# Performance work log

Measured on AMD Instinct MI355X. Metric: run time of the kernel, lower is better.

## Reference

```python
import jax, jax.numpy as jnp
import numpy as np

B, S, H = 4, 2048, 1024

def setup_inputs() -> dict:
    key = jax.random.key(0)
    ks = jax.random.split(key, 4)
    scale = 1.0 / np.sqrt(H)
    x = jax.random.normal(ks[0], (B, S, H), dtype=jnp.float32)
    Wq = jax.random.normal(ks[1], (H, H), dtype=jnp.float32) * scale
    Wk = jax.random.normal(ks[2], (H, H), dtype=jnp.float32) * scale
    Wv = jax.random.normal(ks[3], (H, H), dtype=jnp.float32) * scale
    bq = jnp.zeros((H,), dtype=jnp.float32)
    bk = jnp.zeros((H,), dtype=jnp.float32)
    bv = jnp.zeros((H,), dtype=jnp.float32)
    return {"x": x, "Wq": Wq, "bq": bq, "Wk": Wk, "bk": bk, "Wv": Wv, "bv": bv}

def reference(x, Wq, bq, Wk, bk, Wv, bv):
    # Linear: y = x @ W^T + b (torch nn.Linear convention)
    Q = jnp.einsum('bsh,oh->bso', x, Wq) + bq
    K = jnp.einsum('bsh,oh->bso', x, Wk) + bk
    V = jnp.einsum('bsh,oh->bso', x, Wv) + bv
    scores = jnp.einsum('bqh,bkh->bqk', Q, K) / jnp.sqrt(jnp.float32(H))
    attn = jax.nn.softmax(scores, axis=-1)
    return jnp.einsum('bqk,bkh->bqh', attn, V)
```

## Files before the change

kernel.cpp:

```cpp
#include <hip/hip_runtime.h>
#include <cstdint>
#include <cstddef>


typedef __bf16 bf16;
typedef _Float16 f16;
typedef __bf16 bf16x8 __attribute__((ext_vector_type(8)));
typedef __bf16 bf16x4 __attribute__((ext_vector_type(4)));
typedef _Float16 f16x8 __attribute__((ext_vector_type(8)));
typedef float f32x4 __attribute__((ext_vector_type(4)));

#define LDS_TOTAL 131072

#define XQ (8388608 / 4)
#define WQ (1048576 / 4)
__global__ __launch_bounds__(256)
void cvt_all(const float* __restrict__ x, const float* __restrict__ Wq,
             const float* __restrict__ Wk, const float* __restrict__ Wv,
             bf16* __restrict__ xb, bf16* __restrict__ Wqkv)
{
    const int i = blockIdx.x * 256 + threadIdx.x;
    const float* src;
    bf16* dst;
    if (i < XQ) {
        src = x + 4 * (size_t)i;
        dst = xb + 4 * (size_t)i;
    } else {
        const int j = i - XQ;
        const int w = j / WQ;
        const int off = j - w * WQ;
        const float* ws_ = (w == 0) ? Wq : (w == 1) ? Wk : Wv;
        src = ws_ + 4 * (size_t)off;
        dst = Wqkv + 4 * (size_t)j;
    }
    f32x4 v = *(const f32x4*)src;
    bf16x4 o;
#pragma unroll
    for (int r = 0; r < 4; ++r) o[r] = (bf16)v[r];
    *(bf16x4*)dst = o;
}

#define BM1 128
#define BN1 128
#define BK1 64

__device__ __forceinline__ void stage_tile(const bf16* __restrict__ g, int ld,
                                           bf16* lds_generic, int tid)
{
    auto lds3 = (__attribute__((address_space(3))) char*)lds_generic;
    const int wave = tid >> 6;
#pragma unroll
    for (int issue = 0; issue < 4; ++issue) {
        const int p   = issue * 256 + tid;
        const int row = p >> 3;
        const int cp  = p & 7;
        const int c   = cp ^ (row & 7);
        const bf16* gp = g + (size_t)row * ld + c * 8;
        const unsigned wave_base = (unsigned)(issue * 4096 + wave * 1024);
        __builtin_amdgcn_global_load_lds(
            (const __attribute__((address_space(1))) void*)gp,
            (__attribute__((address_space(3))) void*)(lds3 + wave_base),
            16, 0, 0);
    }
}

__device__ __forceinline__ bf16x8 read_frag(const bf16* lds, int row, int chunk)
{
    const int cp = chunk ^ (row & 7);
    return *(const bf16x8*)(lds + row * BK1 + cp * 8);
}

template <int OUTMODE, int DBUF>
__global__ __launch_bounds__(256, DBUF ? 2 : 4)
void gemm_bt(const bf16* __restrict__ A, const bf16* __restrict__ Bm,
             const float* __restrict__ bias0, const float* __restrict__ bias1,
             const float* __restrict__ bias2, void* __restrict__ C,
             int K, int N, float alpha, long zA, long zB, long zC)
{
    __shared__ alignas(16) bf16 As[DBUF + 1][BM1 * BK1];
    __shared__ alignas(16) bf16 Bs[DBUF + 1][BN1 * BK1];

    const int tid  = threadIdx.x;
    const int lane = tid & 63;
    const int wid  = tid >> 6;
    const int wr   = (wid >> 1) * 64;
    const int wc   = (wid & 1) * 64;
    const int quad = lane >> 4;
    const int l16  = lane & 15;

    const int m0 = blockIdx.y * BM1;
    const int n0 = blockIdx.x * BN1;
    const int z  = blockIdx.z;

    const bf16* Ab = A + (size_t)z * zA + (size_t)m0 * K;
    const bf16* Bb = Bm + (size_t)z * zB + (size_t)n0 * K;

    f32x4 acc[4][4] = {};

    if (DBUF) {
        stage_tile(Ab, K, As[0], tid);
        stage_tile(Bb, K, Bs[0], tid);
    }

    const int niter = K / BK1;
    for (int it = 0; it < niter; ++it) {
        int cur;
        if (DBUF) {
            cur = it & 1;
            __syncthreads();
            if (it + 1 < niter) {
                stage_tile(Ab + (it + 1) * BK1, K, As[cur ^ 1], tid);
                stage_tile(Bb + (it + 1) * BK1, K, Bs[cur ^ 1], tid);
            }
        } else {
            cur = 0;
            __syncthreads();
            stage_tile(Ab + it * BK1, K, As[0], tid);
            stage_tile(Bb + it * BK1, K, Bs[0], tid);
            __syncthreads();
        }
#pragma unroll
        for (int h = 0; h < 2; ++h) {
            bf16x8 af[4], bfr[4];
#pragma unroll
            for (int i = 0; i < 4; ++i)
                af[i]  = read_frag(As[cur], wr + i * 16 + l16, h * 4 + quad);
#pragma unroll
            for (int j = 0; j < 4; ++j)
                bfr[j] = read_frag(Bs[cur], wc + j * 16 + l16, h * 4 + quad);

#pragma unroll
            for (int i = 0; i < 4; ++i)
#pragma unroll
                for (int j = 0; j < 4; ++j)
                    acc[i][j] = __builtin_amdgcn_mfma_f32_16x16x32_bf16(
                        af[i], bfr[j], acc[i][j], 0, 0, 0);
        }
    }

#pragma unroll
    for (int j = 0; j < 4; ++j) {
        const int col3 = n0 + wc + j * 16 + l16;
#pragma unroll
        for (int i = 0; i < 4; ++i) {
            const int rbase = m0 + wr + i * 16 + quad * 4;
            const int mat = col3 >> 10;
            const int col = col3 & 1023;
            const float* bp = (mat == 0) ? bias0 : (mat == 1) ? bias1 : bias2;
            const float bj = bp[col];
            if (mat < 2) {
                bf16* Cb = (bf16*)C + (size_t)mat * (8u << 20);
#pragma unroll
                for (int r = 0; r < 4; ++r)
                    Cb[(size_t)(rbase + r) * 1024 + col] =
                        (bf16)(acc[i][j][r] + bj);
            } else {
                bf16* Cb = (bf16*)C + (size_t)(16u << 20);
                const int b = rbase >> 11;
                const int s = rbase & 2047;
                bf16x4 tmp;
#pragma unroll
                for (int r = 0; r < 4; ++r) tmp[r] = (bf16)(acc[i][j][r] + bj);
                *(bf16x4*)(Cb + (((size_t)((b << 10) + col)) << 11) + s) = tmp;
            }
        }
    }
}

template <int OUTMODE, int NW_N>
__global__ __launch_bounds__(512, 2)
void gemm256(const bf16* __restrict__ A, const bf16* __restrict__ Bm,
             void* __restrict__ C,
             int K, int N, float alpha, long zA, long zB, long zC)
{
    constexpr int MI = 2 * NW_N;
    extern __shared__ __align__(16) char smem[];
    auto lds3 = (__attribute__((address_space(3))) char*)smem;

    const int tid  = threadIdx.x;
    const int lane = tid & 63;
    const int wid  = tid >> 6;
    const int quad = lane >> 4;
    const int l16  = lane & 15;
    const int wc   = (wid % NW_N) * 64;
    const int wr   = (wid / NW_N) * (MI * 16);

    const unsigned gx = gridDim.x, gy = gridDim.y;
    unsigned flat = blockIdx.x + gx * (blockIdx.y + gy * blockIdx.z);
    const unsigned chunk = (gx * gy * gridDim.z) >> 3;
    flat = (flat & 7u) * chunk + (flat >> 3);
    const int bx = flat % gx;
    const unsigned r2 = flat / gx;
    const int by = r2 % gy;
    const int z  = r2 / gy;

    const int m0 = by * 256;
    const int n0 = bx * (NW_N * 64);

    const bf16* Ab = A + (size_t)z * zA + (size_t)m0 * K;
    const bf16* Bb = Bm + (size_t)z * zB + (size_t)n0 * K;

    const int sr  = tid >> 3;
    const int sc  = (tid & 7) ^ (sr & 7);
    const size_t soff = (size_t)sr * K + (size_t)sc * 8;
    const long  hstep = 64L * K;
    const long  h1off = 128L * K;
    const unsigned dmabase = (unsigned)(wid * 1024);

#define STAGE(g, ldsoff)                                                       \
    do {                                                                       \
        __builtin_amdgcn_global_load_lds(                                      \
            (const __attribute__((address_space(1))) void*)((g) + soff),       \
            (__attribute__((address_space(3))) void*)(lds3 + (ldsoff) + dmabase), \
            16, 0, 0);                                                         \
        __builtin_amdgcn_global_load_lds(                                      \
            (const __attribute__((address_space(1))) void*)((g) + soff + hstep), \
            (__attribute__((address_space(3))) void*)(lds3 + (ldsoff) + 8192 + dmabase), \
            16, 0, 0);                                                         \
    } while (0)

    const char* pa = (const char*)smem + (wr + l16) * 128;
    const int x0 = (quad ^ (l16 & 7)) * 16;

    const int NT = K / 64;
    f32x4 acc[MI][4] = {};

    if constexpr (NW_N == 4) {
        const char* pb = (const char*)smem + 65536 + (wc + l16) * 128;
        bf16x8 af[4][2], b01[2][2], b23[2][2];

        STAGE(Ab, 0u);           STAGE(Ab + h1off, 16384u);
        STAGE(Bb, 65536u);       STAGE(Bb + h1off, 65536u + 16384u);
        STAGE(Ab + 64, 32768u);  STAGE(Ab + 64 + h1off, 32768u + 16384u);
        asm volatile("s_waitcnt vmcnt(4)\n\ts_barrier" ::: "memory");

        for (int t = 0; t < NT; ++t) {
            const unsigned d  = (unsigned)(t & 1) * 32768u;
            const unsigned dn = 32768u - d;
            const char* paT = pa + d;
            const char* pbT = pb + d;

#pragma unroll
            for (int i = 0; i < 4; ++i) {
                af[i][0] = *(const bf16x8*)(paT + i * 2048 + x0);
                af[i][1] = *(const bf16x8*)(paT + i * 2048 + (x0 ^ 64));
            }
#pragma unroll
            for (int j = 0; j < 2; ++j) {
                b01[j][0] = *(const bf16x8*)(pbT + j * 2048 + x0);
                b01[j][1] = *(const bf16x8*)(pbT + j * 2048 + (x0 ^ 64));
            }
            if (t + 1 < NT) STAGE(Bb + (t + 1) * 64, 65536u + dn);
            __builtin_amdgcn_s_setprio(1);
#pragma unroll
            for (int i = 0; i < 4; ++i)
#pragma unroll
                for (int j = 0; j < 2; ++j) {
                    acc[i][j] = __builtin_amdgcn_mfma_f32_16x16x32_bf16(
                        af[i][0], b01[j][0], acc[i][j], 0, 0, 0);
                    acc[i][j] = __builtin_amdgcn_mfma_f32_16x16x32_bf16(
                        af[i][1], b01[j][1], acc[i][j], 0, 0, 0);
                }
            __builtin_amdgcn_s_setprio(0);

#pragma unroll
            for (int j = 0; j < 2; ++j) {
                b23[j][0] = *(const bf16x8*)(pbT + (2 + j) * 2048 + x0);
                b23[j][1] = *(const bf16x8*)(pbT + (2 + j) * 2048 + (x0 ^ 64));
            }
            if (t + 1 < NT) STAGE(Bb + (t + 1) * 64 + h1off, 65536u + dn + 16384u);
            __builtin_amdgcn_s_setprio(1);
#pragma unroll
            for (int i = 0; i < 4; ++i)
#pragma unroll
                for (int j = 0; j < 2; ++j) {
                    acc[i][2 + j] = __builtin_amdgcn_mfma_f32_16x16x32_bf16(
                        af[i][0], b23[j][0], acc[i][2 + j], 0, 0, 0);
                    acc[i][2 + j] = __builtin_amdgcn_mfma_f32_16x16x32_bf16(
                        af[i][1], b23[j][1], acc[i][2 + j], 0, 0, 0);
                }
            __builtin_amdgcn_s_setprio(0);

#pragma unroll
            for (int i = 0; i < 4; ++i) {
                af[i][0] = *(const bf16x8*)(paT + (4 + i) * 2048 + x0);
                af[i][1] = *(const bf16x8*)(paT + (4 + i) * 2048 + (x0 ^ 64));
            }
            __builtin_amdgcn_s_setprio(1);
#pragma unroll
            for (int i = 0; i < 4; ++i)
#pragma unroll
                for (int j = 0; j < 2; ++j) {
                    acc[4 + i][2 + j] = __builtin_amdgcn_mfma_f32_16x16x32_bf16(
                        af[i][0], b23[j][0], acc[4 + i][2 + j], 0, 0, 0);
                    acc[4 + i][2 + j] = __builtin_amdgcn_mfma_f32_16x16x32_bf16(
                        af[i][1], b23[j][1], acc[4 + i][2 + j], 0, 0, 0);
                }
            __builtin_amdgcn_s_setprio(0);

            asm volatile("s_barrier" ::: "memory");

#pragma unroll
            for (int j = 0; j < 2; ++j) {
                b01[j][0] = *(const bf16x8*)(pbT + j * 2048 + x0);
                b01[j][1] = *(const bf16x8*)(pbT + j * 2048 + (x0 ^ 64));
            }
            if (t + 2 < NT) {
                STAGE(Ab + (t + 2) * 64, d);
                STAGE(Ab + (t + 2) * 64 + h1off, d + 16384u);
            }
            __builtin_amdgcn_s_setprio(1);
#pragma unroll
            for (int i = 0; i < 4; ++i)
#pragma unroll
                for (int j = 0; j < 2; ++j) {
                    acc[4 + i][j] = __builtin_amdgcn_mfma_f32_16x16x32_bf16(
                        af[i][0], b01[j][0], acc[4 + i][j], 0, 0, 0);
                    acc[4 + i][j] = __builtin_amdgcn_mfma_f32_16x16x32_bf16(
                        af[i][1], b01[j][1], acc[4 + i][j], 0, 0, 0);
                }
            __builtin_amdgcn_s_setprio(0);

            if (t + 2 < NT)
                asm volatile("s_waitcnt vmcnt(4)\n\ts_barrier" ::: "memory");
            else if (t + 1 < NT)
                asm volatile("s_waitcnt vmcnt(0)\n\ts_barrier" ::: "memory");
        }
    } else {
        bf16x8 af[2][2], bfr[4][2];

        STAGE(Ab, 0u);           STAGE(Ab + h1off, 16384u);
        STAGE(Bb, 98304u);
        STAGE(Ab + 64, 32768u);  STAGE(Ab + 64 + h1off, 32768u + 16384u);
        asm volatile("s_waitcnt vmcnt(4)\n\ts_barrier" ::: "memory");

        for (int t = 0; t < NT; ++t) {
            const char* paT = pa + (unsigned)(t % 3) * 32768u;
            const char* pbT = (const char*)smem + 98304u +
                              (unsigned)(t & 1) * 16384u + (wc + l16) * 128;

#pragma unroll
            for (int i = 0; i < 2; ++i) {
                af[i][0] = *(const bf16x8*)(paT + i * 2048 + x0);
                af[i][1] = *(const bf16x8*)(paT + i * 2048 + (x0 ^ 64));
            }
#pragma unroll
            for (int j = 0; j < 4; ++j) {
                bfr[j][0] = *(const bf16x8*)(pbT + j * 2048 + x0);
                bfr[j][1] = *(const bf16x8*)(pbT + j * 2048 + (x0 ^ 64));
            }
            if (t + 1 < NT)
                STAGE(Bb + (t + 1) * 64, 98304u + (unsigned)((t + 1) & 1) * 16384u);
            __builtin_amdgcn_s_setprio(1);
#pragma unroll
            for (int i = 0; i < 2; ++i)
#pragma unroll
                for (int j = 0; j < 4; ++j) {
                    acc[i][j] = __builtin_amdgcn_mfma_f32_16x16x32_bf16(
                        af[i][0], bfr[j][0], acc[i][j], 0, 0, 0);
                    acc[i][j] = __builtin_amdgcn_mfma_f32_16x16x32_bf16(
                        af[i][1], bfr[j][1], acc[i][j], 0, 0, 0);
                }
            __builtin_amdgcn_s_setprio(0);

#pragma unroll
            for (int i = 0; i < 2; ++i) {
                af[i][0] = *(const bf16x8*)(paT + (2 + i) * 2048 + x0);
                af[i][1] = *(const bf16x8*)(paT + (2 + i) * 2048 + (x0 ^ 64));
            }
            if (t + 2 < NT) {
                const unsigned da = (unsigned)((t + 2) % 3) * 32768u;
                STAGE(Ab + (t + 2) * 64, da);
                STAGE(Ab + (t + 2) * 64 + h1off, da + 16384u);
            }
            __builtin_amdgcn_s_setprio(1);
#pragma unroll
            for (int i = 0; i < 2; ++i)
#pragma unroll
                for (int j = 0; j < 4; ++j) {
                    acc[2 + i][j] = __builtin_amdgcn_mfma_f32_16x16x32_bf16(
                        af[i][0], bfr[j][0], acc[2 + i][j], 0, 0, 0);
                    acc[2 + i][j] = __builtin_amdgcn_mfma_f32_16x16x32_bf16(
                        af[i][1], bfr[j][1], acc[2 + i][j], 0, 0, 0);
                }
            __builtin_amdgcn_s_setprio(0);

            if (t + 2 < NT)
                asm volatile("s_waitcnt vmcnt(4)\n\ts_barrier" ::: "memory");
            else if (t + 1 < NT)
                asm volatile("s_waitcnt vmcnt(0)\n\ts_barrier" ::: "memory");
        }
    }
#undef STAGE

#pragma unroll
    for (int j = 0; j < 4; ++j) {
        const int col3 = n0 + wc + j * 16 + l16;
#pragma unroll
        for (int i = 0; i < MI; ++i) {
            const int rbase = m0 + wr + i * 16 + quad * 4;
            if (OUTMODE == 2) {
                f16* Cf = (f16*)C + (size_t)z * zC;
#pragma unroll
                for (int r = 0; r < 4; ++r)
                    Cf[(size_t)(rbase + r) * N + col3] = (f16)(acc[i][j][r] * alpha);
            } else {
                float* Cf = (float*)C + (size_t)z * zC;
#pragma unroll
                for (int r = 0; r < 4; ++r)
                    Cf[(size_t)(rbase + r) * N + col3] = acc[i][j][r];
            }
        }
    }
}

__device__ __forceinline__ float wred_max(float v)
{
#pragma unroll
    for (int o = 32; o > 0; o >>= 1) v = fmaxf(v, __shfl_xor(v, o, 64));
    return v;
}
__device__ __forceinline__ float wred_sum(float v)
{
#pragma unroll
    for (int o = 32; o > 0; o >>= 1) v += __shfl_xor(v, o, 64);
    return v;
}

__global__ __launch_bounds__(256)
void softmax_rows(const f16* __restrict__ Sc, bf16* __restrict__ P)
{
    constexpr int NC = 2048;
    const size_t row = blockIdx.x;
    const f16* src = Sc + row * NC;
    bf16* dst = P + row * NC;
    const int tid = threadIdx.x;

    f16x8 in = *(const f16x8*)(src + tid * 8);
    float v[8];
    float m = -3.4e38f;
#pragma unroll
    for (int i = 0; i < 8; ++i) {
        v[i] = (float)in[i];
        m = fmaxf(m, v[i]);
    }
    m = wred_max(m);

    __shared__ float redm[4], reds[4];
    if ((tid & 63) == 0) redm[tid >> 6] = m;
    __syncthreads();
    m = fmaxf(fmaxf(redm[0], redm[1]), fmaxf(redm[2], redm[3]));

    float s = 0.f;
#pragma unroll
    for (int i = 0; i < 8; ++i) { v[i] = __expf(v[i] - m); s += v[i]; }
    s = wred_sum(s);
    if ((tid & 63) == 0) reds[tid >> 6] = s;
    __syncthreads();
    s = reds[0] + reds[1] + reds[2] + reds[3];

    const float inv = 1.f / s;
    bf16x8 o;
#pragma unroll
    for (int i = 0; i < 8; ++i) o[i] = (bf16)(v[i] * inv);
    *(bf16x8*)(dst + tid * 8) = o;
}

extern "C" void kernel_launch(void* const* d_in, const int* in_sizes, int n_in,
                              void* d_out, int out_size, void* d_ws, size_t ws_size,
                              hipStream_t stream)
{
    constexpr int B = 4, S = 2048, H = 1024;
    const float* x  = (const float*)d_in[0];
    const float* Wq = (const float*)d_in[1];
    const float* bq = (const float*)d_in[2];
    const float* Wk = (const float*)d_in[3];
    const float* bk = (const float*)d_in[4];
    const float* Wv = (const float*)d_in[5];
    const float* bv = (const float*)d_in[6];
    float* out = (float*)d_out;

    char* ws = (char*)d_ws;
    bf16* xb   = (bf16*)ws;
    bf16* Wqkv = (bf16*)(ws + (size_t)(16 << 20));
    bf16* Q    = (bf16*)(ws + (size_t)(22 << 20));
    bf16* Kp   = (bf16*)(ws + (size_t)(38 << 20));
    bf16* Vt   = (bf16*)(ws + (size_t)(54 << 20));
    f16*  Sc   = (f16*) (ws + (size_t)(70 << 20));
    bf16* P    = (bf16*)(ws + (size_t)(22 << 20));

    static bool attr_done = false;
    if (!attr_done) {
        attr_done = true;
        (void)hipFuncSetAttribute(reinterpret_cast<const void*>(gemm256<2, 4>),
                                  hipFuncAttributeMaxDynamicSharedMemorySize,
                                  LDS_TOTAL);
        (void)hipFuncSetAttribute(reinterpret_cast<const void*>(gemm256<3, 2>),
                                  hipFuncAttributeMaxDynamicSharedMemorySize,
                                  LDS_TOTAL);
    }

    dim3 blk(256, 1, 1);
    dim3 blk512(512, 1, 1);

    cvt_all<<<dim3((XQ + 3 * WQ) / 256), blk, 0, stream>>>(
        x, Wq, Wk, Wv, xb, Wqkv);

    gemm_bt<4, 1><<<dim3(3 * H / BN1, (B * S) / BM1, 1), blk, 0, stream>>>(
        xb, Wqkv, bq, bk, bv, Q, H, 3 * H, 1.0f, 0, 0, 0);

    gemm256<2, 4><<<dim3(S / 256, S / 256, B), blk512, LDS_TOTAL, stream>>>(
        Q, Kp, Sc, H, S, 0.03125f,
        (long)S * H, (long)S * H, (long)S * S);

    softmax_rows<<<dim3(B * S), blk, 0, stream>>>(Sc, P);

    gemm256<3, 2><<<dim3(H / 128, S / 256, B), blk512, LDS_TOTAL, stream>>>(
        P, Vt, out, S, H, 1.0f,
        (long)S * S, (long)H * S, (long)S * H);
}
```

Before: 245.3 us.

## Fuse softmax normalization into PV GEMM using precomputed row statistics

The separate softmax kernel that wrote a bf16 probability matrix is replaced by a stats kernel that only computes per-row max and inverse sum. The PV GEMM then loads raw f16 scores, applies exp and normalization in registers, and writes bf16 into LDS before the MFMA loop, with a two-stage buffer. This removes the write and re-read of the full P matrix. The cost is that the exp work is repeated for every column tile of the PV GEMM (8 tiles over H), and A-operand staging becomes register-mediated rather than a direct global-to-LDS DMA. The GEMM templates are also specialized into dedicated kernels.

```diff
diff --git a/kernel.cpp b/kernel.cpp
--- a/kernel.cpp
+++ b/kernel.cpp
@@ -10,7 +10,8 @@
 typedef _Float16 f16x8 __attribute__((ext_vector_type(8)));
 typedef float f32x4 __attribute__((ext_vector_type(4)));
 
-#define LDS_TOTAL 131072
+#define LDS_GEMM256 131072
+#define LDS_PV       98304
 
 #define XQ (8388608 / 4)
 #define WQ (1048576 / 4)
@@ -70,15 +71,13 @@
     return *(const bf16x8*)(lds + row * BK1 + cp * 8);
 }
 
-template <int OUTMODE, int DBUF>
-__global__ __launch_bounds__(256, DBUF ? 2 : 4)
-void gemm_bt(const bf16* __restrict__ A, const bf16* __restrict__ Bm,
-             const float* __restrict__ bias0, const float* __restrict__ bias1,
-             const float* __restrict__ bias2, void* __restrict__ C,
-             int K, int N, float alpha, long zA, long zB, long zC)
-{
-    __shared__ alignas(16) bf16 As[DBUF + 1][BM1 * BK1];
-    __shared__ alignas(16) bf16 Bs[DBUF + 1][BN1 * BK1];
+__global__ __launch_bounds__(256, 2)
+void gemm_qkv(const bf16* __restrict__ A, const bf16* __restrict__ Bm,
+              const float* __restrict__ bias0, const float* __restrict__ bias1,
+              const float* __restrict__ bias2, bf16* __restrict__ C, int K)
+{
+    __shared__ alignas(16) bf16 As[2][BM1 * BK1];
+    __shared__ alignas(16) bf16 Bs[2][BN1 * BK1];
 
     const int tid  = threadIdx.x;
     const int lane = tid & 63;
@@ -90,34 +89,22 @@
 
     const int m0 = blockIdx.y * BM1;
     const int n0 = blockIdx.x * BN1;
-    const int z  = blockIdx.z;
-
-    const bf16* Ab = A + (size_t)z * zA + (size_t)m0 * K;
-    const bf16* Bb = Bm + (size_t)z * zB + (size_t)n0 * K;
+
+    const bf16* Ab = A + (size_t)m0 * K;
+    const bf16* Bb = Bm + (size_t)n0 * K;
 
     f32x4 acc[4][4] = {};
 
-    if (DBUF) {
-        stage_tile(Ab, K, As[0], tid);
-        stage_tile(Bb, K, Bs[0], tid);
-    }
+    stage_tile(Ab, K, As[0], tid);
+    stage_tile(Bb, K, Bs[0], tid);
 
     const int niter = K / BK1;
     for (int it = 0; it < niter; ++it) {
-        int cur;
-        if (DBUF) {
-            cur = it & 1;
-            __syncthreads();
-            if (it + 1 < niter) {
-                stage_tile(Ab + (it + 1) * BK1, K, As[cur ^ 1], tid);
-                stage_tile(Bb + (it + 1) * BK1, K, Bs[cur ^ 1], tid);
-            }
-        } else {
-            cur = 0;
-            __syncthreads();
-            stage_tile(Ab + it * BK1, K, As[0], tid);
-            stage_tile(Bb + it * BK1, K, Bs[0], tid);
-            __syncthreads();
+        const int cur = it & 1;
+        __syncthreads();
+        if (it + 1 < niter) {
+            stage_tile(Ab + (it + 1) * BK1, K, As[cur ^ 1], tid);
+            stage_tile(Bb + (it + 1) * BK1, K, Bs[cur ^ 1], tid);
         }
 #pragma unroll
         for (int h = 0; h < 2; ++h) {
@@ -128,7 +115,6 @@
 #pragma unroll
             for (int j = 0; j < 4; ++j)
                 bfr[j] = read_frag(Bs[cur], wc + j * 16 + l16, h * 4 + quad);
-
 #pragma unroll
             for (int i = 0; i < 4; ++i)
 #pragma unroll
@@ -149,13 +135,13 @@
             const float* bp = (mat == 0) ? bias0 : (mat == 1) ? bias1 : bias2;
             const float bj = bp[col];
             if (mat < 2) {
-                bf16* Cb = (bf16*)C + (size_t)mat * (8u << 20);
+                bf16* Cb = C + (size_t)mat * (8u << 20);
 #pragma unroll
                 for (int r = 0; r < 4; ++r)
                     Cb[(size_t)(rbase + r) * 1024 + col] =
                         (bf16)(acc[i][j][r] + bj);
             } else {
-                bf16* Cb = (bf16*)C + (size_t)(16u << 20);
+                bf16* Cb = C + (size_t)(16u << 20);
                 const int b = rbase >> 11;
                 const int s = rbase & 2047;
                 bf16x4 tmp;
@@ -167,13 +153,11 @@
     }
 }
 
-template <int OUTMODE, int NW_N>
 __global__ __launch_bounds__(512, 2)
-void gemm256(const bf16* __restrict__ A, const bf16* __restrict__ Bm,
-             void* __restrict__ C,
-             int K, int N, float alpha, long zA, long zB, long zC)
-{
-    constexpr int MI = 2 * NW_N;
+void gemm_scores(const bf16* __restrict__ A, const bf16* __restrict__ Bm,
+                 f16* __restrict__ C, int K, int N, float alpha,
+                 long zA, long zB, long zC)
+{
     extern __shared__ __align__(16) char smem[];
     auto lds3 = (__attribute__((address_space(3))) char*)smem;
 
@@ -182,8 +166,8 @@
     const int wid  = tid >> 6;
     const int quad = lane >> 4;
     const int l16  = lane & 15;
-    const int wc   = (wid % NW_N) * 64;
-    const int wr   = (wid / NW_N) * (MI * 16);
+    const int wc   = (wid & 3) * 64;
+    const int wr   = (wid >> 2) * 128;
 
     const unsigned gx = gridDim.x, gy = gridDim.y;
     unsigned flat = blockIdx.x + gx * (blockIdx.y + gy * blockIdx.z);
@@ -195,7 +179,7 @@
     const int z  = r2 / gy;
 
     const int m0 = by * 256;
-    const int n0 = bx * (NW_N * 64);
+    const int n0 = bx * 256;
 
     const bf16* Ab = A + (size_t)z * zA + (size_t)m0 * K;
     const bf16* Bb = Bm + (size_t)z * zB + (size_t)n0 * K;
@@ -220,176 +204,109 @@
     } while (0)
 
     const char* pa = (const char*)smem + (wr + l16) * 128;
+    const char* pb = (const char*)smem + 65536 + (wc + l16) * 128;
     const int x0 = (quad ^ (l16 & 7)) * 16;
 
     const int NT = K / 64;
-    f32x4 acc[MI][4] = {};
-
-    if constexpr (NW_N == 4) {
-        const char* pb = (const char*)smem + 65536 + (wc + l16) * 128;
-        bf16x8 af[4][2], b01[2][2], b23[2][2];
-
-        STAGE(Ab, 0u);           STAGE(Ab + h1off, 16384u);
-        STAGE(Bb, 65536u);       STAGE(Bb + h1off, 65536u + 16384u);
-        STAGE(Ab + 64, 32768u);  STAGE(Ab + 64 + h1off, 32768u + 16384u);
-        asm volatile("s_waitcnt vmcnt(4)\n\ts_barrier" ::: "memory");
-
-        for (int t = 0; t < NT; ++t) {
-            const unsigned d  = (unsigned)(t & 1) * 32768u;
-            const unsigned dn = 32768u - d;
-            const char* paT = pa + d;
-            const char* pbT = pb + d;
-
-#pragma unroll
-            for (int i = 0; i < 4; ++i) {
-                af[i][0] = *(const bf16x8*)(paT + i * 2048 + x0);
-                af[i][1] = *(const bf16x8*)(paT + i * 2048 + (x0 ^ 64));
-            }
+    f32x4 acc[8][4] = {};
+    bf16x8 af[4][2], b01[2][2], b23[2][2];
+
+    STAGE(Ab, 0u);           STAGE(Ab + h1off, 16384u);
+    STAGE(Bb, 65536u);       STAGE(Bb + h1off, 65536u + 16384u);
+    STAGE(Ab + 64, 32768u);  STAGE(Ab + 64 + h1off, 32768u + 16384u);
+    asm volatile("s_waitcnt vmcnt(4)\n\ts_barrier" ::: "memory");
+
+    for (int t = 0; t < NT; ++t) {
+        const unsigned d  = (unsigned)(t & 1) * 32768u;
+        const unsigned dn = 32768u - d;
+        const char* paT = pa + d;
+        const char* pbT = pb + d;
+
+#pragma unroll
+        for (int i = 0; i < 4; ++i) {
+            af[i][0] = *(const bf16x8*)(paT + i * 2048 + x0);
+            af[i][1] = *(const bf16x8*)(paT + i * 2048 + (x0 ^ 64));
+        }
+#pragma unroll
+        for (int j = 0; j < 2; ++j) {
+            b01[j][0] = *(const bf16x8*)(pbT + j * 2048 + x0);
+            b01[j][1] = *(const bf16x8*)(pbT + j * 2048 + (x0 ^ 64));
+        }
+        if (t + 1 < NT) STAGE(Bb + (t + 1) * 64, 65536u + dn);
+        __builtin_amdgcn_s_setprio(1);
+#pragma unroll
+        for (int i = 0; i < 4; ++i)
 #pragma unroll
             for (int j = 0; j < 2; ++j) {
-                b01[j][0] = *(const bf16x8*)(pbT + j * 2048 + x0);
-                b01[j][1] = *(const bf16x8*)(pbT + j * 2048 + (x0 ^ 64));
-            }
-            if (t + 1 < NT) STAGE(Bb + (t + 1) * 64, 65536u + dn);
-            __builtin_amdgcn_s_setprio(1);
-#pragma unroll
-            for (int i = 0; i < 4; ++i)
-#pragma unroll
-                for (int j = 0; j < 2; ++j) {
-                    acc[i][j] = __builtin_amdgcn_mfma_f32_16x16x32_bf16(
-                        af[i][0], b01[j][0], acc[i][j], 0, 0, 0);
-                    acc[i][j] = __builtin_amdgcn_mfma_f32_16x16x32_bf16(
-                        af[i][1], b01[j][1], acc[i][j], 0, 0, 0);
-                }
-            __builtin_amdgcn_s_setprio(0);
-
+                acc[i][j] = __builtin_amdgcn_mfma_f32_16x16x32_bf16(
+                    af[i][0], b01[j][0], acc[i][j], 0, 0, 0);
+                acc[i][j] = __builtin_amdgcn_mfma_f32_16x16x32_bf16(
+                    af[i][1], b01[j][1], acc[i][j], 0, 0, 0);
+            }
+        __builtin_amdgcn_s_setprio(0);
+
+#pragma unroll
+        for (int j = 0; j < 2; ++j) {
+            b23[j][0] = *(const bf16x8*)(pbT + (2 + j) * 2048 + x0);
+            b23[j][1] = *(const bf16x8*)(pbT + (2 + j) * 2048 + (x0 ^ 64));
+        }
+        if (t + 1 < NT) STAGE(Bb + (t + 1) * 64 + h1off, 65536u + dn + 16384u);
+        __builtin_amdgcn_s_setprio(1);
+#pragma unroll
+        for (int i = 0; i < 4; ++i)
 #pragma unroll
             for (int j = 0; j < 2; ++j) {
-                b23[j][0] = *(const bf16x8*)(pbT + (2 + j) * 2048 + x0);
-                b23[j][1] = *(const bf16x8*)(pbT + (2 + j) * 2048 + (x0 ^ 64));
-            }
-            if (t + 1 < NT) STAGE(Bb + (t + 1) * 64 + h1off, 65536u + dn + 16384u);
-            __builtin_amdgcn_s_setprio(1);
-#pragma unroll
-            for (int i = 0; i < 4; ++i)
-#pragma unroll
-                for (int j = 0; j < 2; ++j) {
-                    acc[i][2 + j] = __builtin_amdgcn_mfma_f32_16x16x32_bf16(
-                        af[i][0], b23[j][0], acc[i][2 + j], 0, 0, 0);
-                    acc[i][2 + j] = __builtin_amdgcn_mfma_f32_16x16x32_bf16(
-                        af[i][1], b23[j][1], acc[i][2 + j], 0, 0, 0);
-                }
-            __builtin_amdgcn_s_setprio(0);
-
-#pragma unroll
-            for (int i = 0; i < 4; ++i) {
-                af[i][0] = *(const bf16x8*)(paT + (4 + i) * 2048 + x0);
-                af[i][1] = *(const bf16x8*)(paT + (4 + i) * 2048 + (x0 ^ 64));
-            }
-            __builtin_amdgcn_s_setprio(1);
-#pragma unroll
-            for (int i = 0; i < 4; ++i)
-#pragma unroll
-                for (int j = 0; j < 2; ++j) {
-                    acc[4 + i][2 + j] = __builtin_amdgcn_mfma_f32_16x16x32_bf16(
-                        af[i][0], b23[j][0], acc[4 + i][2 + j], 0, 0, 0);
-                    acc[4 + i][2 + j] = __builtin_amdgcn_mfma_f32_16x16x32_bf16(
-                        af[i][1], b23[j][1], acc[4 + i][2 + j], 0, 0, 0);
-                }
-            __builtin_amdgcn_s_setprio(0);
-
-            asm volatile("s_barrier" ::: "memory");
-
+                acc[i][2 + j] = __builtin_amdgcn_mfma_f32_16x16x32_bf16(
+                    af[i][0], b23[j][0], acc[i][2 + j], 0, 0, 0);
+                acc[i][2 + j] = __builtin_amdgcn_mfma_f32_16x16x32_bf16(
+                    af[i][1], b23[j][1], acc[i][2 + j], 0, 0, 0);
+            }
+        __builtin_amdgcn_s_setprio(0);
+
+#pragma unroll
+        for (int i = 0; i < 4; ++i) {
+            af[i][0] = *(const bf16x8*)(paT + (4 + i) * 2048 + x0);
+            af[i][1] = *(const bf16x8*)(paT + (4 + i) * 2048 + (x0 ^ 64));
+        }
+        __builtin_amdgcn_s_setprio(1);
+#pragma unroll
+        for (int i = 0; i < 4; ++i)
 #pragma unroll
             for (int j = 0; j < 2; ++j) {
-                b01[j][0] = *(const bf16x8*)(pbT + j * 2048 + x0);
-                b01[j][1] = *(const bf16x8*)(pbT + j * 2048 + (x0 ^ 64));
-            }
-            if (t + 2 < NT) {
-                STAGE(Ab + (t + 2) * 64, d);
-                STAGE(Ab + (t + 2) * 64 + h1off, d + 16384u);
-            }
-            __builtin_amdgcn_s_setprio(1);
-#pragma unroll
-            for (int i = 0; i < 4; ++i)
-#pragma unroll
-                for (int j = 0; j < 2; ++j) {
-                    acc[4 + i][j] = __builtin_amdgcn_mfma_f32_16x16x32_bf16(
-                        af[i][0], b01[j][0], acc[4 + i][j], 0, 0, 0);
-                    acc[4 + i][j] = __builtin_amdgcn_mfma_f32_16x16x32_bf16(
-                        af[i][1], b01[j][1], acc[4 + i][j], 0, 0, 0);
-                }
-            __builtin_amdgcn_s_setprio(0);
-
-            if (t + 2 < NT)
-                asm volatile("s_waitcnt vmcnt(4)\n\ts_barrier" ::: "memory");
-            else if (t + 1 < NT)
-                asm volatile("s_waitcnt vmcnt(0)\n\ts_barrier" ::: "memory");
-        }
-    } else {
-        bf16x8 af[2][2], bfr[4][2];
-
-        STAGE(Ab, 0u);           STAGE(Ab + h1off, 16384u);
-        STAGE(Bb, 98304u);
-        STAGE(Ab + 64, 32768u);  STAGE(Ab + 64 + h1off, 32768u + 16384u);
-        asm volatile("s_waitcnt vmcnt(4)\n\ts_barrier" ::: "memory");
-
-        for (int t = 0; t < NT; ++t) {
-            const char* paT = pa + (unsigned)(t % 3) * 32768u;
-            const char* pbT = (const char*)smem + 98304u +
-                              (unsigned)(t & 1) * 16384u + (wc + l16) * 128;
-
-#pragma unroll
-            for (int i = 0; i < 2; ++i) {
-                af[i][0] = *(const bf16x8*)(paT + i * 2048 + x0);
-                af[i][1] = *(const bf16x8*)(paT + i * 2048 + (x0 ^ 64));
-            }
-#pragma unroll
-            for (int j = 0; j < 4; ++j) {
-                bfr[j][0] = *(const bf16x8*)(pbT + j * 2048 + x0);
-                bfr[j][1] = *(const bf16x8*)(pbT + j * 2048 + (x0 ^ 64));
-            }
-            if (t + 1 < NT)
-                STAGE(Bb + (t + 1) * 64, 98304u + (unsigned)((t + 1) & 1) * 16384u);
-            __builtin_amdgcn_s_setprio(1);
-#pragma unroll
-            for (int i = 0; i < 2; ++i)
-#pragma unroll
-                for (int j = 0; j < 4; ++j) {
-                    acc[i][j] = __builtin_amdgcn_mfma_f32_16x16x32_bf16(
-                        af[i][0], bfr[j][0], acc[i][j], 0, 0, 0);
-                    acc[i][j] = __builtin_amdgcn_mfma_f32_16x16x32_bf16(
-                        af[i][1], bfr[j][1], acc[i][j], 0, 0, 0);
-                }
-            __builtin_amdgcn_s_setprio(0);
-
-#pragma unroll
-            for (int i = 0; i < 2; ++i) {
-                af[i][0] = *(const bf16x8*)(paT + (2 + i) * 2048 + x0);
-                af[i][1] = *(const bf16x8*)(paT + (2 + i) * 2048 + (x0 ^ 64));
-            }
-            if (t + 2 < NT) {
-                const unsigned da = (unsigned)((t + 2) % 3) * 32768u;
-                STAGE(Ab + (t + 2) * 64, da);
-                STAGE(Ab + (t + 2) * 64 + h1off, da + 16384u);
-            }
-            __builtin_amdgcn_s_setprio(1);
-#pragma unroll
-            for (int i = 0; i < 2; ++i)
-#pragma unroll
-                for (int j = 0; j < 4; ++j) {
-                    acc[2 + i][j] = __builtin_amdgcn_mfma_f32_16x16x32_bf16(
-                        af[i][0], bfr[j][0], acc[2 + i][j], 0, 0, 0);
-                    acc[2 + i][j] = __builtin_amdgcn_mfma_f32_16x16x32_bf16(
-                        af[i][1], bfr[j][1], acc[2 + i][j], 0, 0, 0);
-                }
-            __builtin_amdgcn_s_setprio(0);
-
-            if (t + 2 < NT)
-                asm volatile("s_waitcnt vmcnt(4)\n\ts_barrier" ::: "memory");
-            else if (t + 1 < NT)
-                asm volatile("s_waitcnt vmcnt(0)\n\ts_barrier" ::: "memory");
-        }
+                acc[4 + i][2 + j] = __builtin_amdgcn_mfma_f32_16x16x32_bf16(
+                    af[i][0], b23[j][0], acc[4 + i][2 + j], 0, 0, 0);
+                acc[4 + i][2 + j] = __builtin_amdgcn_mfma_f32_16x16x32_bf16(
+                    af[i][1], b23[j][1], acc[4 + i][2 + j], 0, 0, 0);
+            }
+        __builtin_amdgcn_s_setprio(0);
+
+        asm volatile("s_barrier" ::: "memory");
+
+#pragma unroll
+        for (int j = 0; j < 2; ++j) {
+            b01[j][0] = *(const bf16x8*)(pbT + j * 2048 + x0);
+            b01[j][1] = *(const bf16x8*)(pbT + j * 2048 + (x0 ^ 64));
+        }
+        if (t + 2 < NT) {
+            STAGE(Ab + (t + 2) * 64, d);
+            STAGE(Ab + (t + 2) * 64 + h1off, d + 16384u);
+        }
+        __builtin_amdgcn_s_setprio(1);
+#pragma unroll
+        for (int i = 0; i < 4; ++i)
+#pragma unroll
+            for (int j = 0; j < 2; ++j) {
+                acc[4 + i][j] = __builtin_amdgcn_mfma_f32_16x16x32_bf16(
+                    af[i][0], b01[j][0], acc[4 + i][j], 0, 0, 0);
+                acc[4 + i][j] = __builtin_amdgcn_mfma_f32_16x16x32_bf16(
+                    af[i][1], b01[j][1], acc[4 + i][j], 0, 0, 0);
+            }
+        __builtin_amdgcn_s_setprio(0);
+
+        if (t + 2 < NT)
+            asm volatile("s_waitcnt vmcnt(4)\n\ts_barrier" ::: "memory");
+        else if (t + 1 < NT)
+            asm volatile("s_waitcnt vmcnt(0)\n\ts_barrier" ::: "memory");
     }
 #undef STAGE
 
@@ -397,19 +314,12 @@
     for (int j = 0; j < 4; ++j) {
         const int col3 = n0 + wc + j * 16 + l16;
 #pragma unroll
-        for (int i = 0; i < MI; ++i) {
+        for (int i = 0; i < 8; ++i) {
             const int rbase = m0 + wr + i * 16 + quad * 4;
-            if (OUTMODE == 2) {
-                f16* Cf = (f16*)C + (size_t)z * zC;
-#pragma unroll
-                for (int r = 0; r < 4; ++r)
-                    Cf[(size_t)(rbase + r) * N + col3] = (f16)(acc[i][j][r] * alpha);
-            } else {
-                float* Cf = (float*)C + (size_t)z * zC;
-#pragma unroll
-                for (int r = 0; r < 4; ++r)
-                    Cf[(size_t)(rbase + r) * N + col3] = acc[i][j][r];
-            }
+            f16* Cf = C + (size_t)z * zC;
+#pragma unroll
+            for (int r = 0; r < 4; ++r)
+                Cf[(size_t)(rbase + r) * N + col3] = (f16)(acc[i][j][r] * alpha);
         }
     }
 }
@@ -428,12 +338,12 @@
 }
 
 __global__ __launch_bounds__(256)
-void softmax_rows(const f16* __restrict__ Sc, bf16* __restrict__ P)
+void stats_rows(const f16* __restrict__ Sc, float* __restrict__ mstat,
+                float* __restrict__ sstat)
 {
     constexpr int NC = 2048;
     const size_t row = blockIdx.x;
     const f16* src = Sc + row * NC;
-    bf16* dst = P + row * NC;
     const int tid = threadIdx.x;
 
     f16x8 in = *(const f16x8*)(src + tid * 8);
@@ -453,17 +363,184 @@
 
     float s = 0.f;
 #pragma unroll
-    for (int i = 0; i < 8; ++i) { v[i] = __expf(v[i] - m); s += v[i]; }
+    for (int i = 0; i < 8; ++i) s += __expf(v[i] - m);
     s = wred_sum(s);
     if ((tid & 63) == 0) reds[tid >> 6] = s;
     __syncthreads();
-    s = reds[0] + reds[1] + reds[2] + reds[3];
-
-    const float inv = 1.f / s;
-    bf16x8 o;
-#pragma unroll
-    for (int i = 0; i < 8; ++i) o[i] = (bf16)(v[i] * inv);
-    *(bf16x8*)(dst + tid * 8) = o;
+    if (tid == 0) {
+        s = reds[0] + reds[1] + reds[2] + reds[3];
+        mstat[row] = m;
+        sstat[row] = 1.f / s;
+    }
+}
+
+__global__ __launch_bounds__(512, 2)
+void pv_fused(const f16* __restrict__ Sc, const bf16* __restrict__ Vt,
+              const float* __restrict__ mstat, const float* __restrict__ sstat,
+              float* __restrict__ out)
+{
+    constexpr int K = 2048, NT = K / 64;
+    extern __shared__ __align__(16) char smem[];
+    auto lds3 = (__attribute__((address_space(3))) char*)smem;
+
+    const int tid  = threadIdx.x;
+    const int lane = tid & 63;
+    const int wid  = tid >> 6;
+    const int quad = lane >> 4;
+    const int l16  = lane & 15;
+    const int wc   = (wid & 1) * 64;
+    const int wr   = (wid >> 1) * 64;
+
+    const unsigned gx = gridDim.x, gy = gridDim.y;
+    unsigned flat = blockIdx.x + gx * (blockIdx.y + gy * blockIdx.z);
+    const unsigned chunkv = (gx * gy * gridDim.z) >> 3;
+    flat = (flat & 7u) * chunkv + (flat >> 3);
+    const int bx = flat % gx;
+    const unsigned r2 = flat / gx;
+    const int by = r2 % gy;
+    const int z  = r2 / gy;
+
+    const int m0 = by * 256;
+    const int n0 = bx * 128;
+
+    const f16*  Ab = Sc + (size_t)z * (2048u * 2048u) + (size_t)m0 * K;
+    const bf16* Bb = Vt + (size_t)z * (1024u * 2048u) + (size_t)n0 * K;
+
+    const int sr  = tid >> 3;
+    const int scB = (tid & 7) ^ (sr & 7);
+    const size_t soffB = (size_t)sr * K + (size_t)scB * 8;
+    const long hstep = 64L * K;
+    const unsigned dmabase = (unsigned)(wid * 1024);
+
+#define STAGE_B(g, ldsoff)                                                     \
+    do {                                                                       \
+        __builtin_amdgcn_global_load_lds(                                      \
+            (const __attribute__((address_space(1))) void*)((g) + soffB),      \
+            (__attribute__((address_space(3))) void*)(lds3 + (ldsoff) + dmabase), \
+            16, 0, 0);                                                         \
+        __builtin_amdgcn_global_load_lds(                                      \
+            (const __attribute__((address_space(1))) void*)((g) + soffB + hstep), \
+            (__attribute__((address_space(3))) void*)(lds3 + (ldsoff) + 8192 + dmabase), \
+            16, 0, 0);                                                         \
+    } while (0)
+
+    const int cA = tid & 7;
+    const int slotA = cA ^ (sr & 7);
+    float mrow[4], isrow[4];
+    {
+        const int rb = z * 2048 + m0 + sr;
+#pragma unroll
+        for (int j = 0; j < 4; ++j) {
+            mrow[j]  = mstat[rb + j * 64];
+            isrow[j] = sstat[rb + j * 64];
+        }
+    }
+    const f16* aldbase = Ab + (size_t)sr * K + cA * 8;
+
+    f16x8 lv[4];
+#define LOAD_A(tt)                                                             \
+    do {                                                                       \
+        const f16* g_ = aldbase + (tt) * 64;                                   \
+        _Pragma("unroll")                                                      \
+        for (int j_ = 0; j_ < 4; ++j_)                                         \
+            lv[j_] = *(const f16x8*)(g_ + (size_t)(j_ * 64) * K);              \
+    } while (0)
+
+#define WRITE_A(bufoff)                                                        \
+    do {                                                                       \
+        _Pragma("unroll")                                                      \
+        for (int j_ = 0; j_ < 4; ++j_) {                                       \
+            bf16x8 o_;                                                         \
+            _Pragma("unroll")                                                  \
+            for (int e_ = 0; e_ < 8; ++e_) {                                   \
+                float vv_ = (float)lv[j_][e_];                                 \
+                o_[e_] = (bf16)(__expf(vv_ - mrow[j_]) * isrow[j_]);           \
+            }                                                                  \
+            *(bf16x8*)((char*)smem + (bufoff) +                                \
+                       (unsigned)((sr + j_ * 64) * 128 + slotA * 16)) = o_;    \
+        }                                                                      \
+    } while (0)
+
+    const char* pa = (const char*)smem + (wr + l16) * 128;
+    const int x0 = (quad ^ (l16 & 7)) * 16;
+
+    f32x4 acc[4][4] = {};
+    bf16x8 af[2][2], bfr[4][2];
+
+    LOAD_A(0);
+    STAGE_B(Bb, 65536u);
+    WRITE_A(0u);
+    asm volatile("s_waitcnt vmcnt(0) lgkmcnt(0)\n\ts_barrier" ::: "memory");
+
+    for (int t = 0; t < NT; ++t) {
+        const unsigned dA = (unsigned)(t & 1) * 32768u;
+        const char* paT = pa + dA;
+        const char* pbT = (const char*)smem + 65536u +
+                          (unsigned)(t & 1) * 16384u + ((wid & 1) * 64 + l16) * 128;
+
+#pragma unroll
+        for (int i = 0; i < 2; ++i) {
+            af[i][0] = *(const bf16x8*)(paT + i * 2048 + x0);
+            af[i][1] = *(const bf16x8*)(paT + i * 2048 + (x0 ^ 64));
+        }
+#pragma unroll
+        for (int j = 0; j < 4; ++j) {
+            bfr[j][0] = *(const bf16x8*)(pbT + j * 2048 + x0);
+            bfr[j][1] = *(const bf16x8*)(pbT + j * 2048 + (x0 ^ 64));
+        }
+        if (t + 1 < NT) {
+            STAGE_B(Bb + (t + 1) * 64, 65536u + (unsigned)((t + 1) & 1) * 16384u);
+            LOAD_A(t + 1);
+        }
+        __builtin_amdgcn_s_setprio(1);
+#pragma unroll
+        for (int i = 0; i < 2; ++i)
+#pragma unroll
+            for (int j = 0; j < 4; ++j) {
+                acc[i][j] = __builtin_amdgcn_mfma_f32_16x16x32_bf16(
+                    af[i][0], bfr[j][0], acc[i][j], 0, 0, 0);
+                acc[i][j] = __builtin_amdgcn_mfma_f32_16x16x32_bf16(
+                    af[i][1], bfr[j][1], acc[i][j], 0, 0, 0);
+            }
+        __builtin_amdgcn_s_setprio(0);
+
+#pragma unroll
+        for (int i = 0; i < 2; ++i) {
+            af[i][0] = *(const bf16x8*)(paT + (2 + i) * 2048 + x0);
+            af[i][1] = *(const bf16x8*)(paT + (2 + i) * 2048 + (x0 ^ 64));
+        }
+        if (t + 1 < NT) WRITE_A((unsigned)((t + 1) & 1) * 32768u);
+        __builtin_amdgcn_s_setprio(1);
+#pragma unroll
+        for (int i = 0; i < 2; ++i)
+#pragma unroll
+            for (int j = 0; j < 4; ++j) {
+                acc[2 + i][j] = __builtin_amdgcn_mfma_f32_16x16x32_bf16(
+                    af[i][0], bfr[j][0], acc[2 + i][j], 0, 0, 0);
+                acc[2 + i][j] = __builtin_amdgcn_mfma_f32_16x16x32_bf16(
+                    af[i][1], bfr[j][1], acc[2 + i][j], 0, 0, 0);
+            }
+        __builtin_amdgcn_s_setprio(0);
+
+        if (t + 1 < NT)
+            asm volatile("s_waitcnt vmcnt(0) lgkmcnt(0)\n\ts_barrier" ::: "memory");
+    }
+#undef STAGE_B
+#undef LOAD_A
+#undef WRITE_A
+
+#pragma unroll
+    for (int j = 0; j < 4; ++j) {
+        const int col3 = n0 + wc + j * 16 + l16;
+#pragma unroll
+        for (int i = 0; i < 4; ++i) {
+            const int rbase = m0 + wr + i * 16 + quad * 4;
+            float* Cf = out + (size_t)z * (2048u * 1024u);
+#pragma unroll
+            for (int r = 0; r < 4; ++r)
+                Cf[(size_t)(rbase + r) * 1024 + col3] = acc[i][j][r];
+        }
+    }
 }
 
 extern "C" void kernel_launch(void* const* d_in, const int* in_sizes, int n_in,
@@ -481,23 +558,24 @@
     float* out = (float*)d_out;
 
     char* ws = (char*)d_ws;
-    bf16* xb   = (bf16*)ws;
-    bf16* Wqkv = (bf16*)(ws + (size_t)(16 << 20));
-    bf16* Q    = (bf16*)(ws + (size_t)(22 << 20));
-    bf16* Kp   = (bf16*)(ws + (size_t)(38 << 20));
-    bf16* Vt   = (bf16*)(ws + (size_t)(54 << 20));
-    f16*  Sc   = (f16*) (ws + (size_t)(70 << 20));
-    bf16* P    = (bf16*)(ws + (size_t)(22 << 20));
+    bf16* xb    = (bf16*)ws;
+    bf16* Wqkv  = (bf16*)(ws + (size_t)(16 << 20));
+    float* mst  = (float*)(ws + (size_t)(22 << 20));
+    float* sst  = (float*)(ws + (size_t)(22 << 20) + 65536);
+    bf16* Q     = (bf16*)(ws + (size_t)(24 << 20));
+    bf16* Kp    = (bf16*)(ws + (size_t)(40 << 20));
+    bf16* Vt    = (bf16*)(ws + (size_t)(56 << 20));
+    f16*  Sc    = (f16*) (ws + (size_t)(72 << 20));
 
     static bool attr_done = false;
     if (!attr_done) {
         attr_done = true;
-        (void)hipFuncSetAttribute(reinterpret_cast<const void*>(gemm256<2, 4>),
+        (void)hipFuncSetAttribute(reinterpret_cast<const void*>(gemm_scores),
                                   hipFuncAttributeMaxDynamicSharedMemorySize,
-                                  LDS_TOTAL);
-        (void)hipFuncSetAttribute(reinterpret_cast<const void*>(gemm256<3, 2>),
+                                  LDS_GEMM256);
+        (void)hipFuncSetAttribute(reinterpret_cast<const void*>(pv_fused),
                                   hipFuncAttributeMaxDynamicSharedMemorySize,
-                                  LDS_TOTAL);
+                                  LDS_PV);
     }
 
     dim3 blk(256, 1, 1);
@@ -506,16 +584,15 @@
     cvt_all<<<dim3((XQ + 3 * WQ) / 256), blk, 0, stream>>>(
         x, Wq, Wk, Wv, xb, Wqkv);
 
-    gemm_bt<4, 1><<<dim3(3 * H / BN1, (B * S) / BM1, 1), blk, 0, stream>>>(
-        xb, Wqkv, bq, bk, bv, Q, H, 3 * H, 1.0f, 0, 0, 0);
-
-    gemm256<2, 4><<<dim3(S / 256, S / 256, B), blk512, LDS_TOTAL, stream>>>(
+    gemm_qkv<<<dim3(3 * H / BN1, (B * S) / BM1, 1), blk, 0, stream>>>(
+        xb, Wqkv, bq, bk, bv, Q, H);
+
+    gemm_scores<<<dim3(S / 256, S / 256, B), blk512, LDS_GEMM256, stream>>>(
         Q, Kp, Sc, H, S, 0.03125f,
         (long)S * H, (long)S * H, (long)S * S);
 
-    softmax_rows<<<dim3(B * S), blk, 0, stream>>>(Sc, P);
-
-    gemm256<3, 2><<<dim3(H / 128, S / 256, B), blk512, LDS_TOTAL, stream>>>(
-        P, Vt, out, S, H, 1.0f,
-        (long)S * S, (long)H * S, (long)S * H);
-}
+    stats_rows<<<dim3(B * S), blk, 0, stream>>>(Sc, mst, sst);
+
+    pv_fused<<<dim3(H / 128, S / 256, B), blk512, LDS_PV, stream>>>(
+        Sc, Vt, mst, sst, out);
+}
```

Result: slower. 270.8 us (+10.4%).
